# Performance work log

Measured on AMD Instinct MI355X. Metric: run time of the kernel, lower is better.

The kernel has to match this reference:

```python
import jax, jax.numpy as jnp
import numpy as np

D = 1024
H = 16
DH = D // H
NEG = -10000000.0


def setup_inputs() -> dict:
    key = jax.random.key(0)
    ks = jax.random.split(key, 12)
    B, L = 2, 2048
    sc = 0.02
    inp = {
        "q": jax.random.normal(ks[0], (B, L, D), jnp.float32),
        "k": jax.random.normal(ks[1], (B, L, D), jnp.float32),
        "v": jax.random.normal(ks[2], (B, L, D), jnp.float32),
        "attention_mask": jax.random.randint(ks[3], (B, L, L), 0, 2) == 1,
        "head_mask": jnp.ones((1, 1, 1), jnp.float32),
        "Wq": sc * jax.random.normal(ks[4], (D, D), jnp.float32),
        "bq": jnp.zeros((D,), jnp.float32),
        "Wk": sc * jax.random.normal(ks[5], (D, D), jnp.float32),
        "bk": jnp.zeros((D,), jnp.float32),
        "Wv": sc * jax.random.normal(ks[6], (D, D), jnp.float32),
        "bv": jnp.zeros((D,), jnp.float32),
        "Wo": sc * jax.random.normal(ks[7], (D, D), jnp.float32),
        "bo": jnp.zeros((D,), jnp.float32),
    }
    return inp


def reference(q, k, v, attention_mask, head_mask, Wq, bq, Wk, bk, Wv, bv, Wo, bo):
    B, Lq, _ = q.shape
    Lk = k.shape[1]
    # QKV projections (nn.Linear: x @ W.T + b), split into heads
    qh = (q @ Wq.T + bq).reshape(B, Lq, H, DH)  # [B,Lq,H,dh]
    kh = (k @ Wk.T + bk).reshape(B, Lk, H, DH)
    vh = (v @ Wv.T + bv).reshape(B, Lk, H, DH)
    # scores [B,H,Lq,Lk], scaled by 1/sqrt(dh)
    scores = jnp.einsum("bihd,bjhd->bhij", qh, kh) / jnp.sqrt(jnp.float32(DH))
    scores = jnp.where(attention_mask[:, None, :, :], NEG, scores)
    probs = jax.nn.softmax(scores, axis=-1)
    probs = probs * head_mask  # broadcastable head mask (dropout is identity in eval)
    ctx = jnp.einsum("bhij,bjhd->bihd", probs, vh).reshape(B, Lq, D)
    # output linear + residual (Add_and_LN with with_lN=False, eval dropout)
    out = ctx @ Wo.T + bo + q
    return out
```

## Files before the change

### kernel.cpp

```cpp
#include <hip/hip_runtime.h>

typedef unsigned short u16;
typedef unsigned long long u64;
typedef __attribute__((ext_vector_type(4))) float f32x4;
typedef __attribute__((ext_vector_type(8))) short s16x8;
typedef __attribute__((ext_vector_type(4))) short s16x4;
typedef __attribute__((ext_vector_type(4))) unsigned int u32x4;
typedef __attribute__((ext_vector_type(2))) unsigned int u32x2;

#define LDS_LOAD16(gp, lp) __builtin_amdgcn_global_load_lds( \
    (__attribute__((address_space(1))) void*)(gp), \
    (__attribute__((address_space(3))) void*)(lp), 16, 0, 0)

#define MFMA16 __builtin_amdgcn_mfma_f32_16x16x32_bf16

constexpr float L2E = 1.44269504088896340736f;

__device__ __forceinline__ u16 f2bf(float x) {
  unsigned u = __float_as_uint(x);
  u += 0x7FFF + ((u >> 16) & 1);
  return (u16)(u >> 16);
}

__device__ __forceinline__ unsigned cvtpk_bf16(float lo, float hi) {
  unsigned r;
  asm("v_cvt_pk_bf16_f32 %0, %1, %2" : "=v"(r) : "v"(lo), "v"(hi));
  return r;
}

struct ConvArgs {
  const float* src[7];
  u16* dst[7];
  int n4[7];
  float scale[7];
};

__global__ __launch_bounds__(256) void convert_many(ConvArgs a) {
  const int arr = blockIdx.y;
  const f32x4* src = (const f32x4*)a.src[arr];
  u16* dst = a.dst[arr];
  const int n4 = a.n4[arr];
  const float sc = a.scale[arr];
  const int stride = gridDim.x * blockDim.x;
  for (int i = blockIdx.x * blockDim.x + threadIdx.x; i < n4; i += stride) {
    f32x4 v = src[i];
    s16x4 o;
#pragma unroll
    for (int j = 0; j < 4; ++j) o[j] = (short)f2bf(v[j] * sc);
    *(s16x4*)(dst + (size_t)i * 4) = o;
  }
}

__global__ __launch_bounds__(256) void mask_to_bits(const unsigned int* __restrict__ m32,
                                                    unsigned long long* __restrict__ bits,
                                                    int n) {
  const int i = blockIdx.x * blockDim.x + threadIdx.x;
  const int lane = threadIdx.x & 63;
  unsigned probe = m32[lane];
  bool bytemode = __any(probe > 1u);
  bool v;
  if (bytemode) v = ((const unsigned char*)m32)[i] != 0;
  else          v = m32[i] != 0;
  unsigned long long b = __ballot(v);
  if (lane == 0) bits[i >> 6] = b;
}

struct QkvArgsB {
  const u16* A[3];
  const u16* B[3];
  const float* bias[3];
  float bscale[3];
  u16* C[3];
};

__global__ __launch_bounds__(256) void gemm_qkv_bf(QkvArgsB a) {
  const int z = blockIdx.z;
  const u16* __restrict__ A = a.A[z];
  const u16* __restrict__ B = a.B[z];
  const float* __restrict__ bias = a.bias[z];
  const float bscale = a.bscale[z];
  u16* __restrict__ C = a.C[z];

  __shared__ u16 As[3][4096];
  __shared__ u16 Bs[3][4096];
  const int tid = threadIdx.x;
  const int lane = tid & 63;
  const int wave = tid >> 6;
  const int g = lane >> 4, c = lane & 15;
  const int g4 = g * 4;
  const int bx = blockIdx.x;
  const int row0 = (((bx & 7) << 2) | (bx >> 3)) * 128;
  const int col0 = blockIdx.y * 128;
  const int wr = (wave >> 1) * 64, wc = (wave & 1) * 64;

  f32x4 acc[4][4] = {};

#define STAGE_QKV(p_, k0_) { _Pragma("unroll") \
    for (int i = 0; i < 2; ++i) { \
      int e = (i * 256 + tid) * 8; \
      LDS_LOAD16(A + (size_t)(row0 + (e >> 5)) * 1024 + (k0_) + (e & 31), As[p_] + e); \
      LDS_LOAD16(B + (size_t)(col0 + (e >> 5)) * 1024 + (k0_) + (e & 31), Bs[p_] + e); } }

  STAGE_QKV(0, 0);
  STAGE_QKV(1, 32);

  for (int s = 0; s < 32; ++s) {
    const int p = s % 3;
    if (s == 31) asm volatile("s_waitcnt vmcnt(0)" ::: "memory");
    else         asm volatile("s_waitcnt vmcnt(4)" ::: "memory");
    __builtin_amdgcn_s_barrier();
    __builtin_amdgcn_sched_barrier(0);
    if (s + 2 < 32) {
      const int np = (s + 2) % 3;
      STAGE_QKV(np, (s + 2) * 32);
    }
    s16x8 af[4], bf[4];
#pragma unroll
    for (int m = 0; m < 4; ++m) af[m] = *(const s16x8*)(As[p] + (wr + m * 16 + c) * 32 + g * 8);
#pragma unroll
    for (int n = 0; n < 4; ++n) bf[n] = *(const s16x8*)(Bs[p] + (wc + n * 16 + c) * 32 + g * 8);
#pragma unroll
    for (int m = 0; m < 4; ++m)
#pragma unroll
      for (int n = 0; n < 4; ++n)
        acc[m][n] = MFMA16(bf[n], af[m], acc[m][n], 0, 0, 0);
  }

  f32x4 bv[4];
#pragma unroll
  for (int n = 0; n < 4; ++n) {
    bv[n] = *(const f32x4*)(bias + col0 + wc + n * 16 + g4);
#pragma unroll
    for (int r = 0; r < 4; ++r) bv[n][r] *= bscale;
  }
#pragma unroll
  for (int m = 0; m < 4; ++m)
#pragma unroll
    for (int n = 0; n < 4; ++n) {
      s16x4 o;
#pragma unroll
      for (int r = 0; r < 4; ++r) o[r] = (short)f2bf(acc[m][n][r] + bv[n][r]);
      *(s16x4*)(C + (size_t)(row0 + wr + m * 16 + c) * 1024 + col0 + wc + n * 16 + g4) = o;
    }
}

struct QkvArgsF {
  const float* A[3];
  const u16* B[3];
  const float* bias[3];
  float bscale[3];
  u16* C[3];
};

__global__ __launch_bounds__(256) void gemm_qkv_f32(QkvArgsF a) {
  const int z = blockIdx.z;
  const float* __restrict__ A = a.A[z];
  const u16* __restrict__ B = a.B[z];
  const float* __restrict__ bias = a.bias[z];
  const float bscale = a.bscale[z];
  u16* __restrict__ C = a.C[z];

  __shared__ u16 As[2][4096];
  __shared__ u16 Bs[2][4096];
  const int tid = threadIdx.x;
  const int lane = tid & 63;
  const int wave = tid >> 6;
  const int g = lane >> 4, c = lane & 15;
  const int g4 = g * 4;
  const int row0 = blockIdx.x * 128;
  const int col0 = blockIdx.y * 128;
  const int wr = (wave >> 1) * 64, wc = (wave & 1) * 64;
  const int ra = tid >> 2;
  const int cca = (tid & 3) * 8;

  f32x4 acc[4][4] = {};
  f32x4 ar[2][2];
#pragma unroll
  for (int i = 0; i < 2; ++i) {
    ar[i][0] = *(const f32x4*)(A + (size_t)(row0 + i * 64 + ra) * 1024 + cca);
    ar[i][1] = *(const f32x4*)(A + (size_t)(row0 + i * 64 + ra) * 1024 + cca + 4);
  }

  for (int s = 0; s < 32; ++s) {
    const int p = s & 1;
    const int k0 = s * 32;
#pragma unroll
    for (int i = 0; i < 2; ++i) {
      unsigned w0 = cvtpk_bf16(ar[i][0][0], ar[i][0][1]);
      unsigned w1 = cvtpk_bf16(ar[i][0][2], ar[i][0][3]);
      unsigned w2 = cvtpk_bf16(ar[i][1][0], ar[i][1][1]);
      unsigned w3 = cvtpk_bf16(ar[i][1][2], ar[i][1][3]);
      union { u32x4 u; s16x8 v; } w;
      w.u = (u32x4){w0, w1, w2, w3};
      *(s16x8*)(As[p] + (i * 256 + tid) * 8) = w.v;
    }
    if (s < 31) {
#pragma unroll
      for (int i = 0; i < 2; ++i) {
        ar[i][0] = *(const f32x4*)(A + (size_t)(row0 + i * 64 + ra) * 1024 + k0 + 32 + cca);
        ar[i][1] = *(const f32x4*)(A + (size_t)(row0 + i * 64 + ra) * 1024 + k0 + 32 + cca + 4);
      }
    }
#pragma unroll
    for (int i = 0; i < 2; ++i) {
      int e = (i * 256 + tid) * 8;
      LDS_LOAD16(B + (size_t)(col0 + (e >> 5)) * 1024 + k0 + (e & 31), Bs[p] + e);
    }
    __syncthreads();

    s16x8 af[4], bf[4];
#pragma unroll
    for (int m = 0; m < 4; ++m) af[m] = *(const s16x8*)(As[p] + (wr + m * 16 + c) * 32 + g * 8);
#pragma unroll
    for (int n = 0; n < 4; ++n) bf[n] = *(const s16x8*)(Bs[p] + (wc + n * 16 + c) * 32 + g * 8);
#pragma unroll
    for (int m = 0; m < 4; ++m)
#pragma unroll
      for (int n = 0; n < 4; ++n)
        acc[m][n] = MFMA16(bf[n], af[m], acc[m][n], 0, 0, 0);
  }

  f32x4 bv[4];
#pragma unroll
  for (int n = 0; n < 4; ++n) {
    bv[n] = *(const f32x4*)(bias + col0 + wc + n * 16 + g4);
#pragma unroll
    for (int r = 0; r < 4; ++r) bv[n][r] *= bscale;
  }
#pragma unroll
  for (int m = 0; m < 4; ++m)
#pragma unroll
    for (int n = 0; n < 4; ++n) {
      s16x4 o;
#pragma unroll
      for (int r = 0; r < 4; ++r) o[r] = (short)f2bf(acc[m][n][r] + bv[n][r]);
      *(s16x4*)(C + (size_t)(row0 + wr + m * 16 + c) * 1024 + col0 + wc + n * 16 + g4) = o;
    }
}

__global__ __launch_bounds__(256) void gemm_out(const u16* __restrict__ A,
                                                const u16* __restrict__ B,
                                                const float* __restrict__ bias,
                                                const float* __restrict__ resid,
                                                float* __restrict__ C) {
  __shared__ u16 As[3][2048];
  __shared__ u16 Bs[3][4096];
  const int tid = threadIdx.x;
  const int lane = tid & 63;
  const int wave = tid >> 6;
  const int g = lane >> 4, c = lane & 15;
  const int g4 = g * 4;
  const int bx = blockIdx.x;
  const int row0 = (((bx & 7) << 3) | (bx >> 3)) * 64;
  const int col0 = blockIdx.y * 128;
  const int wr = (wave >> 1) * 32, wc = (wave & 1) * 64;

  f32x4 acc[2][4] = {};

#define STAGE_OUT(p_, k0_) { \
    LDS_LOAD16(A + (size_t)(row0 + (tid >> 2)) * 1024 + (k0_) + (tid & 3) * 8, As[p_] + tid * 8); \
    _Pragma("unroll") \
    for (int i = 0; i < 2; ++i) { \
      int e = (i * 256 + tid) * 8; \
      LDS_LOAD16(B + (size_t)(col0 + (e >> 5)) * 1024 + (k0_) + (e & 31), Bs[p_] + e); } }

  STAGE_OUT(0, 0);
  STAGE_OUT(1, 32);

  for (int s = 0; s < 32; ++s) {
    const int p = s % 3;
    if (s == 31) asm volatile("s_waitcnt vmcnt(0)" ::: "memory");
    else         asm volatile("s_waitcnt vmcnt(3)" ::: "memory");
    __builtin_amdgcn_s_barrier();
    __builtin_amdgcn_sched_barrier(0);
    if (s + 2 < 32) {
      const int np = (s + 2) % 3;
      STAGE_OUT(np, (s + 2) * 32);
    }
    s16x8 af[2], bf[4];
#pragma unroll
    for (int m = 0; m < 2; ++m) af[m] = *(const s16x8*)(As[p] + (wr + m * 16 + c) * 32 + g * 8);
#pragma unroll
    for (int n = 0; n < 4; ++n) bf[n] = *(const s16x8*)(Bs[p] + (wc + n * 16 + c) * 32 + g * 8);
#pragma unroll
    for (int m = 0; m < 2; ++m)
#pragma unroll
      for (int n = 0; n < 4; ++n)
        acc[m][n] = MFMA16(bf[n], af[m], acc[m][n], 0, 0, 0);
  }

  f32x4 bv[4];
#pragma unroll
  for (int n = 0; n < 4; ++n) bv[n] = *(const f32x4*)(bias + col0 + wc + n * 16 + g4);
#pragma unroll
  for (int m = 0; m < 2; ++m)
#pragma unroll
    for (int n = 0; n < 4; ++n) {
      size_t off = (size_t)(row0 + wr + m * 16 + c) * 1024 + col0 + wc + n * 16 + g4;
      f32x4 rv = *(const f32x4*)(resid + off);
      f32x4 o;
#pragma unroll
      for (int r = 0; r < 4; ++r) o[r] = acc[m][n][r] + bv[n][r] + rv[r];
      *(f32x4*)(C + off) = o;
    }
}

constexpr float NEGV = -10000000.0f;

__global__ __launch_bounds__(256) void attn_kernel(const u16* __restrict__ Qh,
                                                   const u16* __restrict__ Kh,
                                                   const u16* __restrict__ Vh,
                                                   const u64* __restrict__ mbits,
                                                   const float* __restrict__ head_mask,
                                                   u16* __restrict__ ctx) {
  __shared__ u16 Ks[2][4096];
  __shared__ u16 Vt[2][64 * 72];

  const int tid = threadIdx.x;
  const int lane = tid & 63;
  const int wave = tid >> 6;
  const int g = lane >> 4, c = lane & 15;
  const int g4 = g * 4;
  const int wid = (blockIdx.x & 7) * 64 + (blockIdx.x >> 3);
  const int qt = wid & 15;
  const int bh = wid >> 4;
  const int b = bh >> 4;
  const int h = bh & 15;
  const size_t rowbase = (size_t)b * 2048;
  const int D = 1024;

  s16x8 qf[2][2];
#pragma unroll
  for (int s = 0; s < 2; ++s) {
    const int qrow = qt * 128 + s * 64 + wave * 16 + c;
#pragma unroll
    for (int ks = 0; ks < 2; ++ks)
      qf[s][ks] = *(const s16x8*)(Qh + (rowbase + qrow) * D + h * 64 + ks * 32 + g * 8);
  }

  f32x4 accO[2][4] = {};
  float srun[2] = {0.f, 0.f};

  const u64* mrow0 = mbits + (rowbase + qt * 128 + 0 * 64 + wave * 16 + c) * 32;
  const u64* mrow1 = mbits + (rowbase + qt * 128 + 1 * 64 + wave * 16 + c) * 32;

  const int kkK = tid & 63;
  const int aV = tid >> 3;
  const int sV = tid & 7;
  const int dcV = sV * 8;
  const int colV = (2 * aV) ^ (8 * sV);

  const u16* Kbase = Kh + rowbase * D + h * 64;
  const u16* Vbase = Vh + rowbase * D + h * 64;

  s16x8 kreg[2], vreg[2];
#define LOADKV(kb_) { \
    kreg[0] = *(const s16x8*)(Kbase + (size_t)((kb_) + kkK) * D + wave * 8); \
    kreg[1] = *(const s16x8*)(Kbase + (size_t)((kb_) + kkK) * D + (4 + wave) * 8); \
    vreg[0] = *(const s16x8*)(Vbase + (size_t)((kb_) + 2 * aV) * D + dcV); \
    vreg[1] = *(const s16x8*)(Vbase + (size_t)((kb_) + 2 * aV + 1) * D + dcV); }
#define WRITEKV(p_) { \
    *(s16x8*)(Ks[p_] + tid * 8) = kreg[0]; \
    *(s16x8*)(Ks[p_] + 2048 + tid * 8) = kreg[1]; \
    _Pragma("unroll") \
    for (int j = 0; j < 8; ++j) { \
      unsigned pk = (unsigned)(u16)vreg[0][j] | ((unsigned)(u16)vreg[1][j] << 16); \
      *(unsigned*)(Vt[p_] + (dcV + j) * 72 + colV) = pk; } }

  LOADKV(0);
  WRITEKV(0);
  LOADKV(64);
  __syncthreads();

  for (int it = 0; it < 32; ++it) {
    const int p = it & 1;
    if (it < 31) WRITEKV(p ^ 1);
    if (it < 30) LOADKV((it + 2) * 64);

    f32x4 accS[2][4];
    __builtin_amdgcn_s_setprio(1);
#pragma unroll
    for (int t = 0; t < 4; ++t) {
      s16x8 kf0 = *(const s16x8*)(Ks[p] + ((0 + g) * 64 + t * 16 + c) * 8);
      s16x8 kf1 = *(const s16x8*)(Ks[p] + ((4 + g) * 64 + t * 16 + c) * 8);
      f32x4 z0 = {0.f, 0.f, 0.f, 0.f};
      z0 = MFMA16(kf0, qf[0][0], z0, 0, 0, 0);
      accS[0][t] = MFMA16(kf1, qf[0][1], z0, 0, 0, 0);
      f32x4 z1 = {0.f, 0.f, 0.f, 0.f};
      z1 = MFMA16(kf0, qf[1][0], z1, 0, 0, 0);
      accS[1][t] = MFMA16(kf1, qf[1][1], z1, 0, 0, 0);
    }
    __builtin_amdgcn_s_setprio(0);

    s16x8 pa[2][2];
#pragma unroll
    for (int s = 0; s < 2; ++s) {
      u64 mw = (s == 0 ? mrow0 : mrow1)[it];
      u64 sh = mw >> g4;
      unsigned mlo = (unsigned)sh, mhi = (unsigned)(sh >> 32);
      float sp = 0.f;
      unsigned pk0[4], pk1[4];
#pragma unroll
      for (int t = 0; t < 4; ++t) {
        unsigned msrc = (t < 2) ? mlo : mhi;
#pragma unroll
        for (int r = 0; r < 4; ++r) {
          float sv = accS[s][t][r];
          if ((msrc >> ((t & 1) * 16 + r)) & 1) sv = NEGV;
          float pv;
          asm("v_exp_f32 %0, %1" : "=v"(pv) : "v"(sv));
          accS[s][t][r] = pv;
          sp += pv;
        }
        pk0[t] = cvtpk_bf16(accS[s][t][0], accS[s][t][1]);
        pk1[t] = cvtpk_bf16(accS[s][t][2], accS[s][t][3]);
      }
      srun[s] += sp;
#pragma unroll
      for (int ks = 0; ks < 2; ++ks) {
        union { u32x4 u; s16x8 v; } w;
        w.u = (u32x4){pk0[2 * ks], pk1[2 * ks], pk0[2 * ks + 1], pk1[2 * ks + 1]};
        pa[s][ks] = w.v;
      }
    }

    __builtin_amdgcn_s_setprio(1);
#pragma unroll
    for (int d0 = 0; d0 < 4; ++d0) {
      const int dd = d0 * 16 + c;
      const int sw8 = (d0 * 2 + (c >> 3)) * 8;
#pragma unroll
      for (int ks = 0; ks < 2; ++ks) {
        const int base = ks * 32 + g4;
        u32x2 lo = *(const u32x2*)(Vt[p] + dd * 72 + (base ^ sw8));
        u32x2 hi = *(const u32x2*)(Vt[p] + dd * 72 + ((base + 16) ^ sw8));
        union { u32x4 u; s16x8 v; } w;
        w.u = (u32x4){lo[0], lo[1], hi[0], hi[1]};
        accO[0][d0] = MFMA16(w.v, pa[0][ks], accO[0][d0], 0, 0, 0);
        accO[1][d0] = MFMA16(w.v, pa[1][ks], accO[1][d0], 0, 0, 0);
      }
    }
    __builtin_amdgcn_s_setprio(0);
    __syncthreads();
  }

  const float hm = head_mask[0];
#pragma unroll
  for (int s = 0; s < 2; ++s) {
    float tot = srun[s];
    tot += __shfl_xor(tot, 16, 64);
    tot += __shfl_xor(tot, 32, 64);
    float inv = hm / tot;
    const int qrow = qt * 128 + s * 64 + wave * 16 + c;
#pragma unroll
    for (int d0 = 0; d0 < 4; ++d0) {
      s16x4 o;
#pragma unroll
      for (int r = 0; r < 4; ++r) o[r] = (short)f2bf(accO[s][d0][r] * inv);
      *(s16x4*)(ctx + (rowbase + qrow) * D + h * 64 + d0 * 16 + g4) = o;
    }
  }
}

extern "C" void kernel_launch(void* const* d_in, const int* in_sizes, int n_in,
                              void* d_out, int out_size, void* d_ws, size_t ws_size,
                              hipStream_t stream) {
  const float* q  = (const float*)d_in[0];
  const float* k  = (const float*)d_in[1];
  const float* v  = (const float*)d_in[2];
  const void*  am = d_in[3];
  const float* hm = (const float*)d_in[4];
  const float* Wq = (const float*)d_in[5];
  const float* bq = (const float*)d_in[6];
  const float* Wk = (const float*)d_in[7];
  const float* bk = (const float*)d_in[8];
  const float* Wv = (const float*)d_in[9];
  const float* bv = (const float*)d_in[10];
  const float* Wo = (const float*)d_in[11];
  const float* bo = (const float*)d_in[12];

  char* ws = (char*)d_ws;
  const size_t MB = 1024 * 1024;
  const bool big = ws_size >= 58 * MB;

  if (big) {
    u16* qb  = (u16*)(ws + 0 * MB);
    u16* kb  = (u16*)(ws + 8 * MB);
    u16* vb  = (u16*)(ws + 16 * MB);
    u16* wqb = (u16*)(ws + 24 * MB);
    u16* wkb = (u16*)(ws + 26 * MB);
    u16* wvb = (u16*)(ws + 28 * MB);
    u16* wob = (u16*)(ws + 30 * MB);
    u16* Qh  = (u16*)(ws + 32 * MB);
    u16* Kh  = (u16*)(ws + 40 * MB);
    u16* Vh  = (u16*)(ws + 48 * MB);
    unsigned long long* mbits = (unsigned long long*)(ws + 56 * MB);
    u16* ctx = qb;

    ConvArgs ca;
    ca.src[0] = q;  ca.dst[0] = qb;  ca.n4[0] = 1048576; ca.scale[0] = 1.f;
    ca.src[1] = k;  ca.dst[1] = kb;  ca.n4[1] = 1048576; ca.scale[1] = 1.f;
    ca.src[2] = v;  ca.dst[2] = vb;  ca.n4[2] = 1048576; ca.scale[2] = 1.f;
    ca.src[3] = Wq; ca.dst[3] = wqb; ca.n4[3] = 262144;  ca.scale[3] = 0.125f * L2E;
    ca.src[4] = Wk; ca.dst[4] = wkb; ca.n4[4] = 262144;  ca.scale[4] = 1.f;
    ca.src[5] = Wv; ca.dst[5] = wvb; ca.n4[5] = 262144;  ca.scale[5] = 1.f;
    ca.src[6] = Wo; ca.dst[6] = wob; ca.n4[6] = 262144;  ca.scale[6] = 1.f;
    convert_many<<<dim3(512, 7), 256, 0, stream>>>(ca);

    mask_to_bits<<<32768, 256, 0, stream>>>((const unsigned int*)am, mbits, 8388608);

    QkvArgsB ga;
    ga.A[0] = qb; ga.B[0] = wqb; ga.bias[0] = bq; ga.bscale[0] = 0.125f * L2E; ga.C[0] = Qh;
    ga.A[1] = kb; ga.B[1] = wkb; ga.bias[1] = bk; ga.bscale[1] = 1.f;          ga.C[1] = Kh;
    ga.A[2] = vb; ga.B[2] = wvb; ga.bias[2] = bv; ga.bscale[2] = 1.f;          ga.C[2] = Vh;
    gemm_qkv_bf<<<dim3(32, 8, 3), 256, 0, stream>>>(ga);

    attn_kernel<<<512, 256, 0, stream>>>(Qh, Kh, Vh, mbits, hm, ctx);

    gemm_out<<<dim3(64, 8), 256, 0, stream>>>(ctx, wob, bo, q, (float*)d_out);
  } else {
    u16* Qh  = (u16*)(ws + 0 * MB);
    u16* Kh  = (u16*)(ws + 8 * MB);
    u16* Vh  = (u16*)(ws + 16 * MB);
    u16* wqb = (u16*)(ws + 24 * MB);
    u16* wkb = (u16*)(ws + 26 * MB);
    u16* wvb = (u16*)(ws + 28 * MB);
    u16* wob = (u16*)(ws + 30 * MB);
    unsigned long long* mbits = (unsigned long long*)(ws + 32 * MB);
    u16* ctx = (u16*)(ws + 33 * MB);

    ConvArgs ca;
    ca.src[0] = Wq; ca.dst[0] = wqb; ca.n4[0] = 262144; ca.scale[0] = 0.125f * L2E;
    ca.src[1] = Wk; ca.dst[1] = wkb; ca.n4[1] = 262144; ca.scale[1] = 1.f;
    ca.src[2] = Wv; ca.dst[2] = wvb; ca.n4[2] = 262144; ca.scale[2] = 1.f;
    ca.src[3] = Wo; ca.dst[3] = wob; ca.n4[3] = 262144; ca.scale[3] = 1.f;
    convert_many<<<dim3(256, 4), 256, 0, stream>>>(ca);

    mask_to_bits<<<32768, 256, 0, stream>>>((const unsigned int*)am, mbits, 8388608);

    QkvArgsF ga;
    ga.A[0] = q; ga.B[0] = wqb; ga.bias[0] = bq; ga.bscale[0] = 0.125f * L2E; ga.C[0] = Qh;
    ga.A[1] = k; ga.B[1] = wkb; ga.bias[1] = bk; ga.bscale[1] = 1.f;          ga.C[1] = Kh;
    ga.A[2] = v; ga.B[2] = wvb; ga.bias[2] = bv; ga.bscale[2] = 1.f;          ga.C[2] = Vh;
    gemm_qkv_f32<<<dim3(32, 8, 3), 256, 0, stream>>>(ga);

    attn_kernel<<<512, 256, 0, stream>>>(Qh, Kh, Vh, mbits, hm, ctx);

    gemm_out<<<dim3(64, 8), 256, 0, stream>>>(ctx, wob, bo, q, (float*)d_out);
  }
}
```

Measured before the change: 158.8 us.

## Compute softmax row sums with MFMA, hoist V loads, grid-stride mask packing

Result: faster. 149.0 us (-6.1%).

```diff
diff --git a/kernel.cpp b/kernel.cpp
--- a/kernel.cpp
+++ b/kernel.cpp
@@ -54,15 +54,17 @@
 __global__ __launch_bounds__(256) void mask_to_bits(const unsigned int* __restrict__ m32,
                                                     unsigned long long* __restrict__ bits,
                                                     int n) {
-  const int i = blockIdx.x * blockDim.x + threadIdx.x;
   const int lane = threadIdx.x & 63;
   unsigned probe = m32[lane];
   bool bytemode = __any(probe > 1u);
-  bool v;
-  if (bytemode) v = ((const unsigned char*)m32)[i] != 0;
-  else          v = m32[i] != 0;
-  unsigned long long b = __ballot(v);
-  if (lane == 0) bits[i >> 6] = b;
+  const int stride = gridDim.x * blockDim.x;
+  for (int i = blockIdx.x * blockDim.x + threadIdx.x; i < n; i += stride) {
+    bool v;
+    if (bytemode) v = ((const unsigned char*)m32)[i] != 0;
+    else          v = m32[i] != 0;
+    u64 b = __ballot(v);
+    if (lane == 0) bits[i >> 6] = b;
+  }
 }
 
 struct QkvArgsB {
@@ -339,7 +341,11 @@
   }
 
   f32x4 accO[2][4] = {};
-  float srun[2] = {0.f, 0.f};
+  f32x4 accSum[2] = {};
+
+  union { u32x4 u; s16x8 v; } onesu;
+  onesu.u = (u32x4){0x3F803F80u, 0x3F803F80u, 0x3F803F80u, 0x3F803F80u};
+  const s16x8 onesA = onesu.v;
 
   const u64* mrow0 = mbits + (rowbase + qt * 128 + 0 * 64 + wave * 16 + c) * 32;
   const u64* mrow1 = mbits + (rowbase + qt * 128 + 1 * 64 + wave * 16 + c) * 32;
@@ -378,7 +384,6 @@
     if (it < 30) LOADKV((it + 2) * 64);
 
     f32x4 accS[2][4];
-    __builtin_amdgcn_s_setprio(1);
 #pragma unroll
     for (int t = 0; t < 4; ++t) {
       s16x8 kf0 = *(const s16x8*)(Ks[p] + ((0 + g) * 64 + t * 16 + c) * 8);
@@ -390,7 +395,22 @@
       z1 = MFMA16(kf0, qf[1][0], z1, 0, 0, 0);
       accS[1][t] = MFMA16(kf1, qf[1][1], z1, 0, 0, 0);
     }
-    __builtin_amdgcn_s_setprio(0);
+
+    s16x8 vbr[4][2];
+#pragma unroll
+    for (int d0 = 0; d0 < 4; ++d0) {
+      const int dd = d0 * 16 + c;
+      const int sw8 = (d0 * 2 + (c >> 3)) * 8;
+#pragma unroll
+      for (int ks = 0; ks < 2; ++ks) {
+        const int base = ks * 32 + g4;
+        u32x2 lo = *(const u32x2*)(Vt[p] + dd * 72 + (base ^ sw8));
+        u32x2 hi = *(const u32x2*)(Vt[p] + dd * 72 + ((base + 16) ^ sw8));
+        union { u32x4 u; s16x8 v; } w;
+        w.u = (u32x4){lo[0], lo[1], hi[0], hi[1]};
+        vbr[d0][ks] = w.v;
+      }
+    }
 
     s16x8 pa[2][2];
 #pragma unroll
@@ -398,7 +418,6 @@
       u64 mw = (s == 0 ? mrow0 : mrow1)[it];
       u64 sh = mw >> g4;
       unsigned mlo = (unsigned)sh, mhi = (unsigned)(sh >> 32);
-      float sp = 0.f;
       unsigned pk0[4], pk1[4];
 #pragma unroll
       for (int t = 0; t < 4; ++t) {
@@ -410,12 +429,10 @@
           float pv;
           asm("v_exp_f32 %0, %1" : "=v"(pv) : "v"(sv));
           accS[s][t][r] = pv;
-          sp += pv;
         }
         pk0[t] = cvtpk_bf16(accS[s][t][0], accS[s][t][1]);
         pk1[t] = cvtpk_bf16(accS[s][t][2], accS[s][t][3]);
       }
-      srun[s] += sp;
 #pragma unroll
       for (int ks = 0; ks < 2; ++ks) {
         union { u32x4 u; s16x8 v; } w;
@@ -424,33 +441,25 @@
       }
     }
 
-    __builtin_amdgcn_s_setprio(1);
-#pragma unroll
-    for (int d0 = 0; d0 < 4; ++d0) {
-      const int dd = d0 * 16 + c;
-      const int sw8 = (d0 * 2 + (c >> 3)) * 8;
+#pragma unroll
+    for (int d0 = 0; d0 < 4; ++d0)
 #pragma unroll
       for (int ks = 0; ks < 2; ++ks) {
-        const int base = ks * 32 + g4;
-        u32x2 lo = *(const u32x2*)(Vt[p] + dd * 72 + (base ^ sw8));
-        u32x2 hi = *(const u32x2*)(Vt[p] + dd * 72 + ((base + 16) ^ sw8));
-        union { u32x4 u; s16x8 v; } w;
-        w.u = (u32x4){lo[0], lo[1], hi[0], hi[1]};
-        accO[0][d0] = MFMA16(w.v, pa[0][ks], accO[0][d0], 0, 0, 0);
-        accO[1][d0] = MFMA16(w.v, pa[1][ks], accO[1][d0], 0, 0, 0);
+        accO[0][d0] = MFMA16(vbr[d0][ks], pa[0][ks], accO[0][d0], 0, 0, 0);
+        accO[1][d0] = MFMA16(vbr[d0][ks], pa[1][ks], accO[1][d0], 0, 0, 0);
       }
-    }
-    __builtin_amdgcn_s_setprio(0);
+#pragma unroll
+    for (int ks = 0; ks < 2; ++ks) {
+      accSum[0] = MFMA16(onesA, pa[0][ks], accSum[0], 0, 0, 0);
+      accSum[1] = MFMA16(onesA, pa[1][ks], accSum[1], 0, 0, 0);
+    }
     __syncthreads();
   }
 
   const float hm = head_mask[0];
 #pragma unroll
   for (int s = 0; s < 2; ++s) {
-    float tot = srun[s];
-    tot += __shfl_xor(tot, 16, 64);
-    tot += __shfl_xor(tot, 32, 64);
-    float inv = hm / tot;
+    float inv = hm / accSum[s][0];
     const int qrow = qt * 128 + s * 64 + wave * 16 + c;
 #pragma unroll
     for (int d0 = 0; d0 < 4; ++d0) {
@@ -507,7 +516,7 @@
     ca.src[6] = Wo; ca.dst[6] = wob; ca.n4[6] = 262144;  ca.scale[6] = 1.f;
     convert_many<<<dim3(512, 7), 256, 0, stream>>>(ca);
 
-    mask_to_bits<<<32768, 256, 0, stream>>>((const unsigned int*)am, mbits, 8388608);
+    mask_to_bits<<<2048, 256, 0, stream>>>((const unsigned int*)am, mbits, 8388608);
 
     QkvArgsB ga;
     ga.A[0] = qb; ga.B[0] = wqb; ga.bias[0] = bq; ga.bscale[0] = 0.125f * L2E; ga.C[0] = Qh;
@@ -536,7 +545,7 @@
     ca.src[3] = Wo; ca.dst[3] = wob; ca.n4[3] = 262144; ca.scale[3] = 1.f;
     convert_many<<<dim3(256, 4), 256, 0, stream>>>(ca);
 
-    mask_to_bits<<<32768, 256, 0, stream>>>((const unsigned int*)am, mbits, 8388608);
+    mask_to_bits<<<2048, 256, 0, stream>>>((const unsigned int*)am, mbits, 8388608);
 
     QkvArgsF ga;
     ga.A[0] = q; ga.B[0] = wqb; ga.bias[0] = bq; ga.bscale[0] = 0.125f * L2E; ga.C[0] = Qh;
```
